# Performance work log

Hardware: AMD Instinct MI355X
Metric: run time of the kernel (lower is better)

The kernel has to match this reference:

```python
import jax, jax.numpy as jnp
import numpy as np


def l2norm(x):
    return x / jnp.linalg.norm(x, axis=-1, keepdims=True)


def setup_inputs() -> dict:
    key = jax.random.key(0)
    ks = jax.random.split(key, 20)
    B, D, Wd, V, N, L = 384, 1024, 300, 30000, 8000, 16
    s = 1.0 / np.sqrt(D)
    inp = {
        "r": jax.random.normal(ks[0], (B, D), jnp.float32),
        "m": jax.random.normal(ks[1], (B, D), jnp.float32),
        "t": jax.random.normal(ks[2], (B, D), jnp.float32),
        "noun_token_id": jax.random.randint(ks[3], (B, L), 0, V, jnp.int32),
        "noun_len": jax.random.randint(ks[4], (B,), 1, L + 1, jnp.int32),
        "all_nouns_token": jax.random.randint(ks[5], (N,), 0, V, jnp.int32),
        "embed_table": jax.random.normal(ks[6], (V, Wd), jnp.float32) * 0.02,
        "noun_W": jax.random.normal(ks[7], (Wd, D), jnp.float32) / np.sqrt(Wd),
        "noun_b": jnp.zeros((D,), jnp.float32),
        "em_W1": jax.random.normal(ks[8], (D, D), jnp.float32) * s,
        "em_b1": jnp.zeros((D,), jnp.float32),
        "em_W2": jax.random.normal(ks[9], (D, D), jnp.float32) * s,
        "em_b2": jnp.zeros((D,), jnp.float32),
        "tr_W": jax.random.normal(ks[10], (D, D), jnp.float32) * s,
        "tr_b": jnp.zeros((D,), jnp.float32),
    }
    # dict noun_token_id_to_idx as dense map; 0 == missing (torch `if weight_idx:` falsy)
    idx = jax.random.randint(ks[11], (V,), 0, N, jnp.int32)
    present = jax.random.uniform(ks[12], (V,)) < 0.7
    inp["token_to_idx_map"] = jnp.where(present, idx, 0).astype(jnp.int32)
    return inp


def reference(r, m, t, noun_token_id, noun_len, all_nouns_token, token_to_idx_map,
              embed_table, noun_W, noun_b, em_W1, em_b1, em_W2, em_b2, tr_W, tr_b):
    B, D = m.shape
    L = noun_token_id.shape[1]

    # cls_weights = noun_encoder(embed(all_nouns_token))  -> [N, D]
    cls_weights = embed_table[all_nouns_token] @ noun_W + noun_b

    # gen_cpt: vectorized replacement of the per-token python double loop (@no_grad)
    widx = token_to_idx_map[noun_token_id]                # [B, L]
    found = widx > 0                                      # `if weight_idx:` semantics
    mapped = cls_weights[widx]                            # [B, L, D]
    fallback = embed_table[noun_token_id] @ noun_W + noun_b  # noun_encoder(embed(key))
    valid = jnp.arange(L)[None, :] < noun_len[:, None]    # [B, L]
    concepts = jnp.where((found & valid)[..., None], mapped,
                         jnp.where(valid[..., None], fallback, 0.0))
    concepts = jax.lax.stop_gradient(concepts)            # torch.no_grad

    # Attention_EM(m): Linear -> ReLU -> Linear -> Softmax(dim=1)
    h = jax.nn.relu(m @ em_W1 + em_b1)
    A_EM = jax.nn.softmax(h @ em_W2 + em_b2, axis=1)      # [B, D]
    Tr_m = l2norm(m @ tr_W + tr_b)                        # Transform_m

    # EM broadcast: (Tr_m[b] * l2norm(A_EM[b]*t[c])).sum(-1)
    # = ((Tr_m*A_EM)[b] . t[c]) / ||A_EM[b]*t[c]||, expressed as two GEMMs
    num = jnp.einsum('bd,cd->bc', Tr_m * A_EM, t)
    den = jnp.sqrt(jnp.einsum('bd,cd->bc', A_EM * A_EM, t * t))
    EM_score = num / den                                  # [B, B]

    # IS broadcast: cosine(r, t)
    IS_score = l2norm(r) @ l2norm(t).T                    # [B, B]

    score = EM_score + IS_score
    return score, concepts
```

## Files before the change

### kernel.cpp

```cpp
#include <hip/hip_runtime.h>
#include <hip/hip_bf16.h>

#define BDIM 384
#define DDIM 1024
#define LDIM 16
#define WD 300
#define CK 320
#define NROWS (BDIM * LDIM)
#define FELEM (BDIM * DDIM)
#define SELEM (BDIM * BDIM)

typedef __attribute__((ext_vector_type(8))) short short8v;
typedef _Float16 half8 __attribute__((ext_vector_type(8)));
typedef __attribute__((ext_vector_type(4))) float f32x4;

__device__ inline ushort f2bf(float x) {
    union { float f; unsigned u; } c; c.f = x;
    unsigned u = c.u;
    unsigned r = (u + 0x7fffu + ((u >> 16) & 1u)) >> 16;
    return (ushort)r;
}

#define PRE_A 1920
#define PRE_B (PRE_A + 320)
#define PRE_T (PRE_B + 3072)
#define PRE_M (PRE_T + 384)
__global__ __launch_bounds__(256) void prep_all(
    const float* __restrict__ embed, const int* __restrict__ ntid,
    const int* __restrict__ nlen, const int* __restrict__ ant, const int* __restrict__ t2i,
    ushort* __restrict__ Abf, int* __restrict__ rowtok,
    const float* __restrict__ nW, ushort* __restrict__ BbfT,
    const float* __restrict__ W1, const float* __restrict__ W2, const float* __restrict__ W3,
    _Float16* __restrict__ WT1, _Float16* __restrict__ WT2, _Float16* __restrict__ WT3,
    const float* __restrict__ m, _Float16* __restrict__ mh) {
    __shared__ float tile[32][33];
    const int b = blockIdx.x, t = threadIdx.x;

    if (b < PRE_A) {
        int idx = b * 256 + t;
        int row = idx / (CK / 4);
        int q = idx - row * (CK / 4);
        int tok = ntid[row];
        int w = t2i[tok];
        int eff = (w > 0) ? ant[w] : tok;
        bool valid = (row & 15) < nlen[row >> 4];
        if (q == 0) rowtok[row] = valid ? eff : -1;
        ushort4 o = {0, 0, 0, 0};
        if (valid && q < WD / 4) {
            float4 v = *(const float4*)&embed[(size_t)eff * WD + q * 4];
            o.x = f2bf(v.x); o.y = f2bf(v.y); o.z = f2bf(v.z); o.w = f2bf(v.w);
        }
        *(ushort4*)&Abf[(size_t)row * CK + q * 4] = o;
        return;
    }
    if (b < PRE_B) {
        int bb = b - PRE_A;
        const int k0 = (bb % 10) * 32, c0 = (bb / 10) * 32;
        const int r = t >> 3, q = t & 7;
        int k = k0 + r;
        float4 v = {0, 0, 0, 0};
        if (k < WD) v = *(const float4*)&nW[(size_t)k * DDIM + c0 + q * 4];
        tile[r][q * 4 + 0] = v.x; tile[r][q * 4 + 1] = v.y;
        tile[r][q * 4 + 2] = v.z; tile[r][q * 4 + 3] = v.w;
        __syncthreads();
        ushort4 o;
        o.x = f2bf(tile[q * 4 + 0][r]);
        o.y = f2bf(tile[q * 4 + 1][r]);
        o.z = f2bf(tile[q * 4 + 2][r]);
        o.w = f2bf(tile[q * 4 + 3][r]);
        *(ushort4*)&BbfT[(size_t)(c0 + r) * CK + k0 + q * 4] = o;
        return;
    }
    if (b < PRE_T) {
        int bb = b - PRE_B;
        int z = bb >> 10, rem = bb & 1023;
        const float* W = (z == 0) ? W1 : (z == 1) ? W2 : W3;
        _Float16* WT = (z == 0) ? WT1 : (z == 1) ? WT2 : WT3;
        const int k0 = (rem & 31) * 32, c0 = (rem >> 5) * 32;
        const int r = t >> 3, q = t & 7;
        float4 v = *(const float4*)&W[(size_t)(k0 + r) * DDIM + c0 + q * 4];
        tile[r][q * 4 + 0] = v.x; tile[r][q * 4 + 1] = v.y;
        tile[r][q * 4 + 2] = v.z; tile[r][q * 4 + 3] = v.w;
        __syncthreads();
        union { _Float16 h[4]; ushort4 u; } o;
        o.h[0] = (_Float16)tile[q * 4 + 0][r];
        o.h[1] = (_Float16)tile[q * 4 + 1][r];
        o.h[2] = (_Float16)tile[q * 4 + 2][r];
        o.h[3] = (_Float16)tile[q * 4 + 3][r];
        *(ushort4*)&WT[(size_t)(c0 + r) * DDIM + k0 + q * 4] = o.u;
        return;
    }
    {
        int bb = b - PRE_T;
        int i = bb * 1024 + t * 4;
        float4 v = *(const float4*)&m[i];
        union { _Float16 h[4]; ushort4 u; } o;
        o.h[0] = (_Float16)v.x; o.h[1] = (_Float16)v.y;
        o.h[2] = (_Float16)v.z; o.h[3] = (_Float16)v.w;
        *(ushort4*)&mh[i] = o.u;
    }
}

__global__ __launch_bounds__(256) void concepts_mfma(const ushort* __restrict__ Abf,
                                                     const ushort* __restrict__ BbfT,
                                                     const int* __restrict__ rowtok,
                                                     const float* __restrict__ bias,
                                                     float* __restrict__ C) {
    union SMem {
        struct { ushort As[2][128 * 40]; ushort Bs[2][128 * 40]; } g;
        float cst[2][128 * 68];
    };
    __shared__ __align__(16) SMem sm;
    __shared__ int stok[128];

    const int tid = threadIdx.x;
    const int bm = blockIdx.x * 128, bn = blockIdx.y * 128;
    if (tid < 128) stok[tid] = rowtok[bm + tid];

    const int w = tid >> 6, lane = tid & 63;
    const int wrow = (w & 1) * 64, wcol = (w >> 1) * 64;
    const int frow = lane & 15, fk = lane >> 4;
    const int srow = tid >> 2, spart = tid & 3;

    f32x4 acc[4][4];
#pragma unroll
    for (int i = 0; i < 4; ++i)
#pragma unroll
        for (int j = 0; j < 4; ++j) acc[i][j] = (f32x4){0.f, 0.f, 0.f, 0.f};

    int4 pa0, pa1, pb0, pb1;
    constexpr int NK = CK / 32;

#define C_LOAD(ks)                                                                   \
    {                                                                                \
        const int k0_ = (ks) * 32;                                                   \
        pa0 = *(const int4*)&Abf[(size_t)(bm + srow) * CK + k0_ + spart * 8];        \
        pa1 = *(const int4*)&Abf[(size_t)(bm + 64 + srow) * CK + k0_ + spart * 8];   \
        pb0 = *(const int4*)&BbfT[(size_t)(bn + srow) * CK + k0_ + spart * 8];       \
        pb1 = *(const int4*)&BbfT[(size_t)(bn + 64 + srow) * CK + k0_ + spart * 8];  \
    }
#define C_STORE(buf)                                                                 \
    {                                                                                \
        *(int4*)&sm.g.As[buf][srow * 40 + spart * 8] = pa0;                          \
        *(int4*)&sm.g.As[buf][(64 + srow) * 40 + spart * 8] = pa1;                   \
        *(int4*)&sm.g.Bs[buf][srow * 40 + spart * 8] = pb0;                          \
        *(int4*)&sm.g.Bs[buf][(64 + srow) * 40 + spart * 8] = pb1;                   \
    }

    C_LOAD(0);
    C_STORE(0);
    __syncthreads();
    int cur = 0;

    for (int ks = 0; ks < NK; ++ks) {
        if (ks + 1 < NK) C_LOAD(ks + 1);
        short8v a[4], b[4];
#pragma unroll
        for (int i = 0; i < 4; ++i)
            a[i] = *(const short8v*)&sm.g.As[cur][(wrow + i * 16 + frow) * 40 + fk * 8];
#pragma unroll
        for (int j = 0; j < 4; ++j)
            b[j] = *(const short8v*)&sm.g.Bs[cur][(wcol + j * 16 + frow) * 40 + fk * 8];
#pragma unroll
        for (int i = 0; i < 4; ++i)
#pragma unroll
            for (int j = 0; j < 4; ++j)
                acc[i][j] = __builtin_amdgcn_mfma_f32_16x16x32_bf16(a[i], b[j], acc[i][j], 0, 0, 0);
        if (ks + 1 < NK) C_STORE(cur ^ 1);
        __syncthreads();
        cur ^= 1;
    }
#undef C_LOAD
#undef C_STORE

    const int half = w >> 1;
#pragma unroll
    for (int i = 0; i < 4; ++i)
#pragma unroll
        for (int j = 0; j < 4; ++j)
#pragma unroll
            for (int r2 = 0; r2 < 4; ++r2) {
                int row = wrow + i * 16 + fk * 4 + r2;
                int col = j * 16 + frow;
                sm.cst[half][row * 68 + col] = acc[i][j][r2];
            }
    __syncthreads();

#pragma unroll
    for (int it = 0; it < 16; ++it) {
        int f = it * 256 + tid;
        int seg = f & 15;
        int rowh = f >> 4;
        int h2 = rowh >> 7, row = rowh & 127;
        float4 o = *(const float4*)&sm.cst[h2][row * 68 + seg * 4];
        int colb = h2 * 64 + seg * 4;
        float4 bv = *(const float4*)&bias[bn + colb];
        bool zero = (stok[row] < 0);
        o.x = zero ? 0.f : o.x + bv.x;
        o.y = zero ? 0.f : o.y + bv.y;
        o.z = zero ? 0.f : o.z + bv.z;
        o.w = zero ? 0.f : o.w + bv.w;
        *(float4*)&C[(size_t)(bm + row) * DDIM + bn + colb] = o;
    }
}

template <int MODE>
__device__ __forceinline__ void emgemm_body(const _Float16* __restrict__ Ah,
                                            const _Float16* __restrict__ WT,
                                            const float* __restrict__ bias,
                                            float* __restrict__ outF,
                                            _Float16* __restrict__ outH) {
    __shared__ __align__(16) _Float16 As[2][32 * 72];
    __shared__ __align__(16) _Float16 Bs[2][32 * 72];
    const int tid = threadIdx.x;
    const int bm = blockIdx.x * 32, bn = blockIdx.y * 32;
    const int lane = tid & 63;
    const int wrow = (tid >> 6) * 16;
    const int frow = lane & 15, fk = lane >> 4;
    const int srow = tid >> 2, spart = tid & 3;

    f32x4 acc0 = {0.f, 0.f, 0.f, 0.f}, acc1 = {0.f, 0.f, 0.f, 0.f};
    int4 pa0, pa1, pb0, pb1;
    constexpr int NK = DDIM / 64;

#define E_LOAD(ks)                                                                  \
    {                                                                               \
        const int k0_ = (ks) * 64 + spart * 16;                                     \
        pa0 = *(const int4*)&Ah[(size_t)(bm + srow) * DDIM + k0_];                  \
        pa1 = *(const int4*)&Ah[(size_t)(bm + srow) * DDIM + k0_ + 8];              \
        pb0 = *(const int4*)&WT[(size_t)(bn + srow) * DDIM + k0_];                  \
        pb1 = *(const int4*)&WT[(size_t)(bn + srow) * DDIM + k0_ + 8];              \
    }
#define E_STORE(buf)                                                                \
    {                                                                               \
        *(int4*)&As[buf][srow * 72 + spart * 16] = pa0;                             \
        *(int4*)&As[buf][srow * 72 + spart * 16 + 8] = pa1;                         \
        *(int4*)&Bs[buf][srow * 72 + spart * 16] = pb0;                             \
        *(int4*)&Bs[buf][srow * 72 + spart * 16 + 8] = pb1;                         \
    }

    E_LOAD(0);
    E_STORE(0);
    __syncthreads();
    int cur = 0;

    for (int ks = 0; ks < NK; ++ks) {
        if (ks + 1 < NK) E_LOAD(ks + 1);
#pragma unroll
        for (int kk = 0; kk < 2; ++kk) {
            half8 a = *(const half8*)&As[cur][(wrow + frow) * 72 + kk * 32 + fk * 8];
            half8 b0 = *(const half8*)&Bs[cur][frow * 72 + kk * 32 + fk * 8];
            half8 b1 = *(const half8*)&Bs[cur][(16 + frow) * 72 + kk * 32 + fk * 8];
            acc0 = __builtin_amdgcn_mfma_f32_16x16x32_f16(a, b0, acc0, 0, 0, 0);
            acc1 = __builtin_amdgcn_mfma_f32_16x16x32_f16(a, b1, acc1, 0, 0, 0);
        }
        if (ks + 1 < NK) E_STORE(cur ^ 1);
        __syncthreads();
        cur ^= 1;
    }
#undef E_LOAD
#undef E_STORE

    const int orow0 = bm + wrow + fk * 4;
    const int c0 = bn + frow, c1 = bn + 16 + frow;
    const float b0v = bias[c0], b1v = bias[c1];
#pragma unroll
    for (int r = 0; r < 4; ++r) {
        int row = orow0 + r;
        float v0 = acc0[r] + b0v;
        float v1 = acc1[r] + b1v;
        if (MODE == 1) {
            outH[(size_t)row * DDIM + c0] = (_Float16)fmaxf(v0, 0.f);
            outH[(size_t)row * DDIM + c1] = (_Float16)fmaxf(v1, 0.f);
        } else {
            outF[(size_t)row * DDIM + c0] = v0;
            outF[(size_t)row * DDIM + c1] = v1;
        }
    }
}

__global__ __launch_bounds__(128) void emgemm13(const _Float16* __restrict__ mh,
                                                const _Float16* __restrict__ WT1,
                                                const _Float16* __restrict__ WT3,
                                                const float* __restrict__ b1,
                                                const float* __restrict__ b3,
                                                _Float16* __restrict__ hh,
                                                float* __restrict__ Tr) {
    if (blockIdx.z == 0)
        emgemm_body<1>(mh, WT1, b1, nullptr, hh);
    else
        emgemm_body<0>(mh, WT3, b3, Tr, nullptr);
}

__global__ __launch_bounds__(128) void emgemm2(const _Float16* __restrict__ hh,
                                               const _Float16* __restrict__ WT2,
                                               const float* __restrict__ b2,
                                               float* __restrict__ S2) {
    emgemm_body<0>(hh, WT2, b2, S2, nullptr);
}

__device__ inline float bred_sum(float x, float* sbuf) {
#pragma unroll
    for (int off = 32; off; off >>= 1) x += __shfl_down(x, off);
    __syncthreads();
    if ((threadIdx.x & 63) == 0) sbuf[threadIdx.x >> 6] = x;
    __syncthreads();
    return sbuf[0] + sbuf[1] + sbuf[2] + sbuf[3];
}
__device__ inline float bred_max(float x, float* sbuf) {
#pragma unroll
    for (int off = 32; off; off >>= 1) x = fmaxf(x, __shfl_down(x, off));
    __syncthreads();
    if ((threadIdx.x & 63) == 0) sbuf[threadIdx.x >> 6] = x;
    __syncthreads();
    return fmaxf(fmaxf(sbuf[0], sbuf[1]), fmaxf(sbuf[2], sbuf[3]));
}

__global__ __launch_bounds__(256) void rowops(const float* __restrict__ S2,
                                              const float* __restrict__ Tr,
                                              const float* __restrict__ rr,
                                              const float* __restrict__ tt,
                                              _Float16* __restrict__ uh, _Float16* __restrict__ vh,
                                              _Float16* __restrict__ rh, _Float16* __restrict__ th,
                                              _Float16* __restrict__ t2h,
                                              float* __restrict__ inv_r,
                                              float* __restrict__ inv_t) {
    __shared__ float sbuf[4];
    const int b = blockIdx.x, tid = threadIdx.x;
    const size_t base = (size_t)b * DDIM + tid * 4;

    const float4 s4 = *(const float4*)&S2[base];
    float mx = fmaxf(fmaxf(s4.x, s4.y), fmaxf(s4.z, s4.w));
    mx = bred_max(mx, sbuf);
    float e0 = expf(s4.x - mx), e1 = expf(s4.y - mx), e2 = expf(s4.z - mx), e3 = expf(s4.w - mx);
    float sum = bred_sum(e0 + e1 + e2 + e3, sbuf);
    float invsum = 1.f / sum;

    const float4 tr4 = *(const float4*)&Tr[base];
    float ss = tr4.x * tr4.x + tr4.y * tr4.y + tr4.z * tr4.z + tr4.w * tr4.w;
    ss = bred_sum(ss, sbuf);
    float invn = 1.f / sqrtf(ss);

    float a0 = e0 * invsum, a1 = e1 * invsum, a2 = e2 * invsum, a3 = e3 * invsum;
    union { _Float16 h[4]; ushort4 u; } o;

    o.h[0] = (_Float16)(tr4.x * invn * a0 * 1024.f);
    o.h[1] = (_Float16)(tr4.y * invn * a1 * 1024.f);
    o.h[2] = (_Float16)(tr4.z * invn * a2 * 1024.f);
    o.h[3] = (_Float16)(tr4.w * invn * a3 * 1024.f);
    *(ushort4*)&uh[base] = o.u;

    float q0 = a0 * 32.f, q1 = a1 * 32.f, q2 = a2 * 32.f, q3 = a3 * 32.f;
    o.h[0] = (_Float16)(q0 * q0); o.h[1] = (_Float16)(q1 * q1);
    o.h[2] = (_Float16)(q2 * q2); o.h[3] = (_Float16)(q3 * q3);
    *(ushort4*)&vh[base] = o.u;

    const float4 r4 = *(const float4*)&rr[base];
    o.h[0] = (_Float16)r4.x; o.h[1] = (_Float16)r4.y;
    o.h[2] = (_Float16)r4.z; o.h[3] = (_Float16)r4.w;
    *(ushort4*)&rh[base] = o.u;

    const float4 t4 = *(const float4*)&tt[base];
    o.h[0] = (_Float16)t4.x; o.h[1] = (_Float16)t4.y;
    o.h[2] = (_Float16)t4.z; o.h[3] = (_Float16)t4.w;
    *(ushort4*)&th[base] = o.u;

    o.h[0] = (_Float16)(t4.x * t4.x); o.h[1] = (_Float16)(t4.y * t4.y);
    o.h[2] = (_Float16)(t4.z * t4.z); o.h[3] = (_Float16)(t4.w * t4.w);
    *(ushort4*)&t2h[base] = o.u;

    float sr = bred_sum(r4.x * r4.x + r4.y * r4.y + r4.z * r4.z + r4.w * r4.w, sbuf);
    float st = bred_sum(t4.x * t4.x + t4.y * t4.y + t4.z * t4.z + t4.w * t4.w, sbuf);
    if (tid == 0) {
        inv_r[b] = 1.f / sqrtf(sr);
        inv_t[b] = 1.f / sqrtf(st);
    }
}

__global__ __launch_bounds__(128) void score_mfma(const _Float16* __restrict__ uh,
                                                  const _Float16* __restrict__ vh,
                                                  const _Float16* __restrict__ rh,
                                                  const _Float16* __restrict__ th,
                                                  const _Float16* __restrict__ t2h,
                                                  const float* __restrict__ inv_r,
                                                  const float* __restrict__ inv_t,
                                                  float* __restrict__ out) {
    __shared__ __align__(16) _Float16 Us[2][32 * 72];
    __shared__ __align__(16) _Float16 Vs[2][32 * 72];
    __shared__ __align__(16) _Float16 Rs[2][32 * 72];
    __shared__ __align__(16) _Float16 Ts[2][32 * 72];
    __shared__ __align__(16) _Float16 Qs[2][32 * 72];

    const int tid = threadIdx.x;
    const int bm = blockIdx.x * 32, bn = blockIdx.y * 32;
    const int lane = tid & 63;
    const int wrow = (tid >> 6) * 16;
    const int frow = lane & 15, fk = lane >> 4;
    const int srow = tid >> 2, spart = tid & 3;

    f32x4 an0 = {0.f, 0.f, 0.f, 0.f}, an1 = an0;
    f32x4 ad0 = an0, ad1 = an0, ai0 = an0, ai1 = an0;
    int4 pu0, pu1, pv0, pv1, pr0, pr1, pt0, pt1, pq0, pq1;
    constexpr int NK = DDIM / 64;

#define S_LOAD(ks)                                                                   \
    {                                                                                \
        const size_t mo = (size_t)(bm + srow) * DDIM + (ks) * 64 + spart * 16;       \
        const size_t no = (size_t)(bn + srow) * DDIM + (ks) * 64 + spart * 16;       \
        pu0 = *(const int4*)&uh[mo];  pu1 = *(const int4*)&uh[mo + 8];               \
        pv0 = *(const int4*)&vh[mo];  pv1 = *(const int4*)&vh[mo + 8];               \
        pr0 = *(const int4*)&rh[mo];  pr1 = *(const int4*)&rh[mo + 8];               \
        pt0 = *(const int4*)&th[no];  pt1 = *(const int4*)&th[no + 8];               \
        pq0 = *(const int4*)&t2h[no]; pq1 = *(const int4*)&t2h[no + 8];              \
    }
#define S_STORE(buf)                                                                 \
    {                                                                                \
        const int lo = srow * 72 + spart * 16;                                       \
        *(int4*)&Us[buf][lo] = pu0; *(int4*)&Us[buf][lo + 8] = pu1;                  \
        *(int4*)&Vs[buf][lo] = pv0; *(int4*)&Vs[buf][lo + 8] = pv1;                  \
        *(int4*)&Rs[buf][lo] = pr0; *(int4*)&Rs[buf][lo + 8] = pr1;                  \
        *(int4*)&Ts[buf][lo] = pt0; *(int4*)&Ts[buf][lo + 8] = pt1;                  \
        *(int4*)&Qs[buf][lo] = pq0; *(int4*)&Qs[buf][lo + 8] = pq1;                  \
    }

    S_LOAD(0);
    S_STORE(0);
    __syncthreads();
    int cur = 0;

    for (int ks = 0; ks < NK; ++ks) {
        if (ks + 1 < NK) S_LOAD(ks + 1);
#pragma unroll
        for (int kk = 0; kk < 2; ++kk) {
            const int ao = (wrow + frow) * 72 + kk * 32 + fk * 8;
            const int bo0 = frow * 72 + kk * 32 + fk * 8;
            const int bo1 = (16 + frow) * 72 + kk * 32 + fk * 8;
            half8 au = *(const half8*)&Us[cur][ao];
            half8 av = *(const half8*)&Vs[cur][ao];
            half8 ar = *(const half8*)&Rs[cur][ao];
            half8 bt0 = *(const half8*)&Ts[cur][bo0];
            half8 bt1 = *(const half8*)&Ts[cur][bo1];
            half8 bq0 = *(const half8*)&Qs[cur][bo0];
            half8 bq1 = *(const half8*)&Qs[cur][bo1];
            an0 = __builtin_amdgcn_mfma_f32_16x16x32_f16(au, bt0, an0, 0, 0, 0);
            an1 = __builtin_amdgcn_mfma_f32_16x16x32_f16(au, bt1, an1, 0, 0, 0);
            ad0 = __builtin_amdgcn_mfma_f32_16x16x32_f16(av, bq0, ad0, 0, 0, 0);
            ad1 = __builtin_amdgcn_mfma_f32_16x16x32_f16(av, bq1, ad1, 0, 0, 0);
            ai0 = __builtin_amdgcn_mfma_f32_16x16x32_f16(ar, bt0, ai0, 0, 0, 0);
            ai1 = __builtin_amdgcn_mfma_f32_16x16x32_f16(ar, bt1, ai1, 0, 0, 0);
        }
        if (ks + 1 < NK) S_STORE(cur ^ 1);
        __syncthreads();
        cur ^= 1;
    }
#undef S_LOAD
#undef S_STORE

    const int orow0 = bm + wrow + fk * 4;
    const int c0 = bn + frow, c1 = bn + 16 + frow;
    const float it0 = inv_t[c0], it1 = inv_t[c1];
#pragma unroll
    for (int r = 0; r < 4; ++r) {
        int row = orow0 + r;
        float ir = inv_r[row];
        float em0 = an0[r] / (32.f * sqrtf(ad0[r]));
        float em1 = an1[r] / (32.f * sqrtf(ad1[r]));
        out[(size_t)row * BDIM + c0] = em0 + ai0[r] * ir * it0;
        out[(size_t)row * BDIM + c1] = em1 + ai1[r] * ir * it1;
    }
}

extern "C" void kernel_launch(void* const* d_in, const int* in_sizes, int n_in, void* d_out,
                              int out_size, void* d_ws, size_t ws_size, hipStream_t stream) {
    const float* r = (const float*)d_in[0];
    const float* m = (const float*)d_in[1];
    const float* t = (const float*)d_in[2];
    const int* ntid = (const int*)d_in[3];
    const int* nlen = (const int*)d_in[4];
    const int* ant = (const int*)d_in[5];
    const float* embed = (const float*)d_in[6];
    const float* noun_W = (const float*)d_in[7];
    const float* noun_b = (const float*)d_in[8];
    const float* em_W1 = (const float*)d_in[9];
    const float* em_b1 = (const float*)d_in[10];
    const float* em_W2 = (const float*)d_in[11];
    const float* em_b2 = (const float*)d_in[12];
    const float* tr_W = (const float*)d_in[13];
    const float* tr_b = (const float*)d_in[14];
    const int* t2i = (const int*)d_in[15];

    float* score = (float*)d_out;
    float* concepts = score + (size_t)SELEM;

    char* base = (char*)d_ws;
    size_t off = 0;
    auto alloc = [&](size_t bytes) { char* p = base + off; off += (bytes + 255) & ~(size_t)255; return p; };
    int* rowtok = (int*)alloc(NROWS * 4);
    float* inv_r = (float*)alloc(BDIM * 4);
    float* inv_t = (float*)alloc(BDIM * 4);
    ushort* Abf = (ushort*)alloc((size_t)NROWS * CK * 2);
    ushort* BbfT = (ushort*)alloc((size_t)DDIM * CK * 2);
    _Float16* WT1 = (_Float16*)alloc((size_t)DDIM * DDIM * 2);
    _Float16* WT2 = (_Float16*)alloc((size_t)DDIM * DDIM * 2);
    _Float16* WT3 = (_Float16*)alloc((size_t)DDIM * DDIM * 2);
    _Float16* mh = (_Float16*)alloc((size_t)FELEM * 2);
    _Float16* hh = (_Float16*)alloc((size_t)FELEM * 2);
    float* S2 = (float*)alloc((size_t)FELEM * 4);
    float* Tr = (float*)alloc((size_t)FELEM * 4);
    _Float16* uh = (_Float16*)alloc((size_t)FELEM * 2);
    _Float16* vh = (_Float16*)alloc((size_t)FELEM * 2);
    _Float16* rh = (_Float16*)alloc((size_t)FELEM * 2);
    _Float16* th = (_Float16*)alloc((size_t)FELEM * 2);
    _Float16* t2h = (_Float16*)alloc((size_t)FELEM * 2);

    prep_all<<<PRE_M, 256, 0, stream>>>(embed, ntid, nlen, ant, t2i, Abf, rowtok,
                                        noun_W, BbfT, em_W1, em_W2, tr_W, WT1, WT2, WT3,
                                        m, mh);

    dim3 gC(NROWS / 128, DDIM / 128);
    concepts_mfma<<<gC, 256, 0, stream>>>(Abf, BbfT, rowtok, noun_b, concepts);

    dim3 g13(BDIM / 32, DDIM / 32, 2);
    emgemm13<<<g13, 128, 0, stream>>>(mh, WT1, WT3, em_b1, tr_b, hh, Tr);

    dim3 gG(BDIM / 32, DDIM / 32);
    emgemm2<<<gG, 128, 0, stream>>>(hh, WT2, em_b2, S2);

    rowops<<<BDIM, 256, 0, stream>>>(S2, Tr, r, t, uh, vh, rh, th, t2h, inv_r, inv_t);

    dim3 gS(BDIM / 32, BDIM / 32);
    score_mfma<<<gS, 128, 0, stream>>>(uh, vh, rh, th, t2h, inv_r, inv_t, score);
}
```

Before: 59.39 us.

## Co-schedule concepts GEMM tiles alongside EM GEMM2 and rowops kernels

The separate concepts GEMM launch is removed. Its 384 tiles are split across two heterogeneous kernels: 192 run as extra blocks of the EM second-GEMM launch and 192 as extra blocks of the rowops launch. The independent concepts work fills idle CUs left by the small dependent-chain kernels, and one launch disappears. GEMM2 is also rewritten as a 256-thread, 4-wave 32x32 tile with K-step 64. All blocks now reserve the large 70KB shared buffer, which lowers occupancy for the lighter roles.

```diff
diff --git a/kernel.cpp b/kernel.cpp
--- a/kernel.cpp
+++ b/kernel.cpp
@@ -101,20 +101,18 @@
     }
 }
 
-__global__ __launch_bounds__(256) void concepts_mfma(const ushort* __restrict__ Abf,
-                                                     const ushort* __restrict__ BbfT,
-                                                     const int* __restrict__ rowtok,
-                                                     const float* __restrict__ bias,
-                                                     float* __restrict__ C) {
-    union SMem {
-        struct { ushort As[2][128 * 40]; ushort Bs[2][128 * 40]; } g;
-        float cst[2][128 * 68];
-    };
-    __shared__ __align__(16) SMem sm;
-    __shared__ int stok[128];
+__device__ __forceinline__ void concepts_role(int cu, const ushort* __restrict__ Abf,
+                                              const ushort* __restrict__ BbfT,
+                                              const int* __restrict__ rowtok,
+                                              const float* __restrict__ nbias,
+                                              float* __restrict__ C, char* smem) {
+    ushort* CAs = (ushort*)smem;
+    ushort* CBs = (ushort*)(smem + 20480);
+    float*  cst = (float*)smem;
+    int* stok = (int*)(smem + 69632);
 
     const int tid = threadIdx.x;
-    const int bm = blockIdx.x * 128, bn = blockIdx.y * 128;
+    const int bm = (cu % 48) * 128, bn = (cu / 48) * 128;
     if (tid < 128) stok[tid] = rowtok[bm + tid];
 
     const int w = tid >> 6, lane = tid & 63;
@@ -141,10 +139,10 @@
     }
 #define C_STORE(buf)                                                                 \
     {                                                                                \
-        *(int4*)&sm.g.As[buf][srow * 40 + spart * 8] = pa0;                          \
-        *(int4*)&sm.g.As[buf][(64 + srow) * 40 + spart * 8] = pa1;                   \
-        *(int4*)&sm.g.Bs[buf][srow * 40 + spart * 8] = pb0;                          \
-        *(int4*)&sm.g.Bs[buf][(64 + srow) * 40 + spart * 8] = pb1;                   \
+        *(int4*)&CAs[(buf) * 5120 + srow * 40 + spart * 8] = pa0;                    \
+        *(int4*)&CAs[(buf) * 5120 + (64 + srow) * 40 + spart * 8] = pa1;             \
+        *(int4*)&CBs[(buf) * 5120 + srow * 40 + spart * 8] = pb0;                    \
+        *(int4*)&CBs[(buf) * 5120 + (64 + srow) * 40 + spart * 8] = pb1;             \
     }
 
     C_LOAD(0);
@@ -157,10 +155,10 @@
         short8v a[4], b[4];
 #pragma unroll
         for (int i = 0; i < 4; ++i)
-            a[i] = *(const short8v*)&sm.g.As[cur][(wrow + i * 16 + frow) * 40 + fk * 8];
+            a[i] = *(const short8v*)&CAs[cur * 5120 + (wrow + i * 16 + frow) * 40 + fk * 8];
 #pragma unroll
         for (int j = 0; j < 4; ++j)
-            b[j] = *(const short8v*)&sm.g.Bs[cur][(wcol + j * 16 + frow) * 40 + fk * 8];
+            b[j] = *(const short8v*)&CBs[cur * 5120 + (wcol + j * 16 + frow) * 40 + fk * 8];
 #pragma unroll
         for (int i = 0; i < 4; ++i)
 #pragma unroll
@@ -182,7 +180,7 @@
             for (int r2 = 0; r2 < 4; ++r2) {
                 int row = wrow + i * 16 + fk * 4 + r2;
                 int col = j * 16 + frow;
-                sm.cst[half][row * 68 + col] = acc[i][j][r2];
+                cst[half * 8704 + row * 68 + col] = acc[i][j][r2];
             }
     __syncthreads();
 
@@ -192,9 +190,9 @@
         int seg = f & 15;
         int rowh = f >> 4;
         int h2 = rowh >> 7, row = rowh & 127;
-        float4 o = *(const float4*)&sm.cst[h2][row * 68 + seg * 4];
+        float4 o = *(const float4*)&cst[h2 * 8704 + row * 68 + seg * 4];
         int colb = h2 * 64 + seg * 4;
-        float4 bv = *(const float4*)&bias[bn + colb];
+        float4 bv = *(const float4*)&nbias[bn + colb];
         bool zero = (stok[row] < 0);
         o.x = zero ? 0.f : o.x + bv.x;
         o.y = zero ? 0.f : o.y + bv.y;
@@ -292,14 +290,84 @@
         emgemm_body<0>(mh, WT3, b3, Tr, nullptr);
 }
 
-__global__ __launch_bounds__(128) void emgemm2(const _Float16* __restrict__ hh,
-                                               const _Float16* __restrict__ WT2,
-                                               const float* __restrict__ b2,
-                                               float* __restrict__ S2) {
-    emgemm_body<0>(hh, WT2, b2, S2, nullptr);
-}
-
-__device__ inline float bred_sum(float x, float* sbuf) {
+__device__ __forceinline__ void em2_body256(const _Float16* __restrict__ Ah,
+                                            const _Float16* __restrict__ WT,
+                                            const float* __restrict__ bias,
+                                            float* __restrict__ outF,
+                                            int bm, int bn,
+                                            _Float16* As, _Float16* Bs) {
+    const int tid = threadIdx.x;
+    const int lane = tid & 63;
+    const int w = tid >> 6;
+    const int hr = (w & 1) * 16, hc = (w >> 1) * 16;
+    const int frow = lane & 15, fk = lane >> 4;
+    const int srow = tid >> 3, spart = tid & 7;
+
+    f32x4 acc = {0.f, 0.f, 0.f, 0.f};
+    int4 pa, pb;
+    constexpr int NK = DDIM / 64;
+
+#define E2_LOAD(ks)                                                                 \
+    {                                                                               \
+        const int k0_ = (ks) * 64 + spart * 8;                                      \
+        pa = *(const int4*)&Ah[(size_t)(bm + srow) * DDIM + k0_];                   \
+        pb = *(const int4*)&WT[(size_t)(bn + srow) * DDIM + k0_];                   \
+    }
+#define E2_STORE(buf)                                                               \
+    {                                                                               \
+        *(int4*)&As[(buf) * 2304 + srow * 72 + spart * 8] = pa;                     \
+        *(int4*)&Bs[(buf) * 2304 + srow * 72 + spart * 8] = pb;                     \
+    }
+
+    E2_LOAD(0);
+    E2_STORE(0);
+    __syncthreads();
+    int cur = 0;
+
+    for (int ks = 0; ks < NK; ++ks) {
+        if (ks + 1 < NK) E2_LOAD(ks + 1);
+#pragma unroll
+        for (int kk = 0; kk < 2; ++kk) {
+            half8 a = *(const half8*)&As[cur * 2304 + (hr + frow) * 72 + kk * 32 + fk * 8];
+            half8 b = *(const half8*)&Bs[cur * 2304 + (hc + frow) * 72 + kk * 32 + fk * 8];
+            acc = __builtin_amdgcn_mfma_f32_16x16x32_f16(a, b, acc, 0, 0, 0);
+        }
+        if (ks + 1 < NK) E2_STORE(cur ^ 1);
+        __syncthreads();
+        cur ^= 1;
+    }
+#undef E2_LOAD
+#undef E2_STORE
+
+    const int col = bn + hc + frow;
+    const float bv = bias[col];
+#pragma unroll
+    for (int r2 = 0; r2 < 4; ++r2) {
+        int row = bm + hr + fk * 4 + r2;
+        outF[(size_t)row * DDIM + col] = acc[r2] + bv;
+    }
+}
+
+__global__ __launch_bounds__(256) void emc(const _Float16* __restrict__ hh,
+                                           const _Float16* __restrict__ WT2,
+                                           const float* __restrict__ b2,
+                                           float* __restrict__ S2,
+                                           const ushort* __restrict__ Abf,
+                                           const ushort* __restrict__ BbfT,
+                                           const int* __restrict__ rowtok,
+                                           const float* __restrict__ nbias,
+                                           float* __restrict__ C) {
+    __shared__ __align__(16) char smem[69632 + 512];
+    const int blk = blockIdx.x;
+    if (blk < 384) {
+        int bm = (blk % 12) * 32, bn = (blk / 12) * 32;
+        em2_body256(hh, WT2, b2, S2, bm, bn, (_Float16*)smem, (_Float16*)(smem + 9216));
+    } else {
+        concepts_role(blk - 384, Abf, BbfT, rowtok, nbias, C, smem);
+    }
+}
+
+__device__ __forceinline__ float bred_sum(float x, float* sbuf) {
 #pragma unroll
     for (int off = 32; off; off >>= 1) x += __shfl_down(x, off);
     __syncthreads();
@@ -307,7 +375,7 @@
     __syncthreads();
     return sbuf[0] + sbuf[1] + sbuf[2] + sbuf[3];
 }
-__device__ inline float bred_max(float x, float* sbuf) {
+__device__ __forceinline__ float bred_max(float x, float* sbuf) {
 #pragma unroll
     for (int off = 32; off; off >>= 1) x = fmaxf(x, __shfl_down(x, off));
     __syncthreads();
@@ -316,17 +384,16 @@
     return fmaxf(fmaxf(sbuf[0], sbuf[1]), fmaxf(sbuf[2], sbuf[3]));
 }
 
-__global__ __launch_bounds__(256) void rowops(const float* __restrict__ S2,
-                                              const float* __restrict__ Tr,
-                                              const float* __restrict__ rr,
-                                              const float* __restrict__ tt,
-                                              _Float16* __restrict__ uh, _Float16* __restrict__ vh,
-                                              _Float16* __restrict__ rh, _Float16* __restrict__ th,
-                                              _Float16* __restrict__ t2h,
-                                              float* __restrict__ inv_r,
-                                              float* __restrict__ inv_t) {
-    __shared__ float sbuf[4];
-    const int b = blockIdx.x, tid = threadIdx.x;
+__device__ __forceinline__ void rowops_body(const float* __restrict__ S2,
+                                            const float* __restrict__ Tr,
+                                            const float* __restrict__ rr,
+                                            const float* __restrict__ tt,
+                                            _Float16* __restrict__ uh, _Float16* __restrict__ vh,
+                                            _Float16* __restrict__ rh, _Float16* __restrict__ th,
+                                            _Float16* __restrict__ t2h,
+                                            float* __restrict__ inv_r, float* __restrict__ inv_t,
+                                            int b, float* sbuf) {
+    const int tid = threadIdx.x;
     const size_t base = (size_t)b * DDIM + tid * 4;
 
     const float4 s4 = *(const float4*)&S2[base];
@@ -374,6 +441,28 @@
     if (tid == 0) {
         inv_r[b] = 1.f / sqrtf(sr);
         inv_t[b] = 1.f / sqrtf(st);
+    }
+}
+
+__global__ __launch_bounds__(256) void rowc(const float* __restrict__ S2,
+                                            const float* __restrict__ Tr,
+                                            const float* __restrict__ rr,
+                                            const float* __restrict__ tt,
+                                            _Float16* __restrict__ uh, _Float16* __restrict__ vh,
+                                            _Float16* __restrict__ rh, _Float16* __restrict__ th,
+                                            _Float16* __restrict__ t2h,
+                                            float* __restrict__ inv_r, float* __restrict__ inv_t,
+                                            const ushort* __restrict__ Abf,
+                                            const ushort* __restrict__ BbfT,
+                                            const int* __restrict__ rowtok,
+                                            const float* __restrict__ nbias,
+                                            float* __restrict__ C) {
+    __shared__ __align__(16) char smem[69632 + 512];
+    const int blk = blockIdx.x;
+    if (blk < 384) {
+        rowops_body(S2, Tr, rr, tt, uh, vh, rh, th, t2h, inv_r, inv_t, blk, (float*)smem);
+    } else {
+        concepts_role(blk - 384 + 192, Abf, BbfT, rowtok, nbias, C, smem);
     }
 }
 
@@ -517,16 +606,13 @@
                                         noun_W, BbfT, em_W1, em_W2, tr_W, WT1, WT2, WT3,
                                         m, mh);
 
-    dim3 gC(NROWS / 128, DDIM / 128);
-    concepts_mfma<<<gC, 256, 0, stream>>>(Abf, BbfT, rowtok, noun_b, concepts);
-
     dim3 g13(BDIM / 32, DDIM / 32, 2);
     emgemm13<<<g13, 128, 0, stream>>>(mh, WT1, WT3, em_b1, tr_b, hh, Tr);
 
-    dim3 gG(BDIM / 32, DDIM / 32);
-    emgemm2<<<gG, 128, 0, stream>>>(hh, WT2, em_b2, S2);
-
-    rowops<<<BDIM, 256, 0, stream>>>(S2, Tr, r, t, uh, vh, rh, th, t2h, inv_r, inv_t);
+    emc<<<576, 256, 0, stream>>>(hh, WT2, em_b2, S2, Abf, BbfT, rowtok, noun_b, concepts);
+
+    rowc<<<576, 256, 0, stream>>>(S2, Tr, r, t, uh, vh, rh, th, t2h, inv_r, inv_t,
+                                  Abf, BbfT, rowtok, noun_b, concepts);
 
     dim3 gS(BDIM / 32, BDIM / 32);
     score_mfma<<<gS, 128, 0, stream>>>(uh, vh, rh, th, t2h, inv_r, inv_t, score);
```

Measured after the change: 63.98 us. 1.08x slower.
